# Kernel optimization log

Measured on AMD Instinct MI355X. Metric: run time of the kernel, lower is better.

## Reference

```python
import jax, jax.numpy as jnp
import numpy as np

B, C, H, W = 8, 512, 64, 64
CDIV = 8
CFG = C // CDIV  # f/g channels = 64


def setup_inputs() -> dict:
    key = jax.random.key(0)
    ks = jax.random.split(key, 8)
    x = jax.random.normal(ks[0], (B, C, H, W), dtype=jnp.float32)
    # 1x1 conv weights (spectral-norm omitted: weights used as-given), orthogonal-ish small init
    Wf = jax.random.normal(ks[1], (CFG, C), dtype=jnp.float32) * 0.02
    bf = jnp.zeros((CFG,), dtype=jnp.float32)
    Wg = jax.random.normal(ks[2], (CFG, C), dtype=jnp.float32) * 0.02
    bg = jnp.zeros((CFG,), dtype=jnp.float32)
    Wh = jax.random.normal(ks[3], (C, C), dtype=jnp.float32) * 0.02
    bh = jnp.zeros((C,), dtype=jnp.float32)
    # module inits gamma=0 (identity output); use 0.5 so the attention path is exercised
    gamma = jnp.float32(0.5)
    return {"x": x, "Wf": Wf, "bf": bf, "Wg": Wg, "bg": bg, "Wh": Wh, "bh": bh, "gamma": gamma}


def reference(x, Wf, bf, Wg, bg, Wh, bh, gamma):
    Bb, Cc, Hh, Ww = x.shape
    N = Hh * Ww
    xf = x.reshape(Bb, Cc, N)  # [B, C, N]
    # 1x1 convs == per-pixel linear maps
    f = jnp.einsum('oc,bcn->bon', Wf, xf) + bf[:, None]  # [B, CFG, N]
    g = jnp.einsum('oc,bcn->bon', Wg, xf) + bg[:, None]  # [B, CFG, N]
    h = jnp.einsum('oc,bcn->bon', Wh, xf) + bh[:, None]  # [B, C, N]
    # attention scores over spatial tokens: queries g, keys f -> [B, N, N]
    s = jnp.einsum('bci,bcj->bij', g, f)
    beta = jax.nn.softmax(s, axis=-1)
    o = jnp.einsum('bij,bcj->bci', beta, h).reshape(Bb, Cc, Hh, Ww)
    return gamma * o + x
```

## Files before the change

kernel.cpp:

```cpp
#include <hip/hip_runtime.h>
#include <hip/hip_bf16.h>

typedef __bf16 bf16;
typedef __attribute__((ext_vector_type(2))) __bf16 bf16x2;
typedef __attribute__((ext_vector_type(4))) __bf16 bf16x4;
typedef __attribute__((ext_vector_type(8))) __bf16 bf16x8;
typedef __attribute__((ext_vector_type(4))) float f32x4;
typedef long long i64;
typedef unsigned char u8;

#define MFMA16x16x32 __builtin_amdgcn_mfma_f32_16x16x32_bf16
#define MFMA_FP8 __builtin_amdgcn_mfma_f32_16x16x32_fp8_fp8

#define NB 8
#define NC 512
#define NN 4096
#define CFG 64

#define XP 520
#define TP 74

#define EXP_OFF 4.5f

__global__ __launch_bounds__(256) void k_wprep(
    const float* __restrict__ Wf, const float* __restrict__ bfv,
    const float* __restrict__ Wg, const float* __restrict__ bgv,
    const float* __restrict__ Wh,
    bf16* __restrict__ Wfg, bf16* __restrict__ Whb, float* __restrict__ bfg)
{
    int idx = blockIdx.x * 256 + threadIdx.x;
    if (idx < 32768)       Wfg[idx] = (bf16)Wf[idx];
    else if (idx < 65536)  Wfg[idx] = (bf16)Wg[idx - 32768];
    if (idx < 262144)      Whb[idx] = (bf16)Wh[idx];
    if (idx < 64)          bfg[idx] = bfv[idx];
    else if (idx < 128)    bfg[idx] = bgv[idx - 64];
}

__global__ __launch_bounds__(512) void k_fused(
    const float* __restrict__ x, const bf16* __restrict__ Wfg,
    const float* __restrict__ bfg, const bf16* __restrict__ Whb,
    const float* __restrict__ bh,
    bf16* __restrict__ fF, bf16* __restrict__ gF, u8* __restrict__ hT)
{
    __shared__ bf16 X[64 * XP];
    __shared__ bf16 tile[64 * TP];

    int b = blockIdx.x, n0 = blockIdx.y * 64;
    int t = threadIdx.x;

    for (int cc = 0; cc < 8; cc++) {
        int cl = t >> 3, seg = (t & 7) * 8;
        const float* src = x + ((size_t)(b * NC + cc * 64 + cl)) * NN + n0 + seg;
        float4 v0 = ((const float4*)src)[0];
        float4 v1 = ((const float4*)src)[1];
        bf16* tr = &tile[cl * TP + seg];
        *(bf16x2*)(tr + 0) = bf16x2{(bf16)v0.x, (bf16)v0.y};
        *(bf16x2*)(tr + 2) = bf16x2{(bf16)v0.z, (bf16)v0.w};
        *(bf16x2*)(tr + 4) = bf16x2{(bf16)v1.x, (bf16)v1.y};
        *(bf16x2*)(tr + 6) = bf16x2{(bf16)v1.z, (bf16)v1.w};
        __syncthreads();
        int nl = t >> 3, cs = (t & 7) * 8;
        bf16 buf[8];
#pragma unroll
        for (int u = 0; u < 8; u++) buf[u] = tile[(cs + u) * TP + nl];
        *(bf16x8*)&X[nl * XP + cc * 64 + cs] = *(bf16x8*)buf;
        __syncthreads();
    }

    int w = t >> 6, l = t & 63;
    int lr = l & 15, lq = l >> 4;

    {
        const bf16* Ab = Whb + (size_t)(w * 64) * NC;
        f32x4 acc[4][4] = {};
        for (int k0 = 0; k0 < NC; k0 += 32) {
            bf16x8 a[4], bb[4];
#pragma unroll
            for (int fi = 0; fi < 4; fi++)
                a[fi] = *(const bf16x8*)(Ab + (size_t)(fi*16 + lr) * NC + k0 + lq*8);
#pragma unroll
            for (int fj = 0; fj < 4; fj++)
                bb[fj] = *(const bf16x8*)&X[(fj*16 + lr) * XP + k0 + lq*8];
#pragma unroll
            for (int fi = 0; fi < 4; fi++)
#pragma unroll
                for (int fj = 0; fj < 4; fj++)
                    acc[fi][fj] = MFMA16x16x32(a[fi], bb[fj], acc[fi][fj], 0, 0, 0);
        }
#pragma unroll
        for (int fi = 0; fi < 4; fi++)
#pragma unroll
            for (int fj = 0; fj < 4; fj++)
#pragma unroll
                for (int tt = 0; tt < 4; tt++) {
                    int c = w*64 + fi*16 + lq*4 + tt;
                    int j = n0 + fj*16 + lr;
                    float v = acc[fi][fj][tt] + bh[c];
                    int jt = j >> 6, ks = (j >> 5) & 1, lqd = (j >> 3) & 3, e = j & 7;
                    int ct = c >> 4, crd = c & 15;
                    size_t off = ((((size_t)(b*64 + jt)*32 + ct)*2 + ks)*64 + (lqd*16 + crd))*8 + e;
                    int pk = __builtin_amdgcn_cvt_pk_fp8_f32(v, v, 0, false);
                    hT[off] = (u8)pk;
                }
    }

    {
        const bf16* Bb = Wfg + (size_t)(w * 16) * NC;
        f32x4 acc2[4] = {};
        for (int k0 = 0; k0 < NC; k0 += 32) {
            bf16x8 a[4], bo;
#pragma unroll
            for (int fi = 0; fi < 4; fi++)
                a[fi] = *(const bf16x8*)&X[(fi*16 + lr) * XP + k0 + lq*8];
            bo = *(const bf16x8*)(Bb + (size_t)lr * NC + k0 + lq*8);
#pragma unroll
            for (int fi = 0; fi < 4; fi++)
                acc2[fi] = MFMA16x16x32(a[fi], bo, acc2[fi], 0, 0, 0);
        }
#pragma unroll
        for (int fi = 0; fi < 4; fi++)
#pragma unroll
            for (int tt = 0; tt < 4; tt++) {
                int n = n0 + fi*16 + lq*4 + tt;
                int o = w*16 + lr;
                float v = acc2[fi][tt] + bfg[o];
                int c = o & 63;
                bf16* dst = (o < 64) ? fF : gF;
                int jt16 = n >> 4, nr = n & 15;
                int ks = c >> 5, lqd = (c >> 3) & 3, e = c & 7;
                size_t off = (((size_t)(b*256 + jt16)*2 + ks)*64 + (lqd*16 + nr))*8 + e;
                dst[off] = (bf16)v;
            }
    }
}

__global__ __launch_bounds__(1024, 4) void k_attn(
    const bf16* __restrict__ fF, const bf16* __restrict__ gF,
    const u8* __restrict__ hT, const float* __restrict__ x,
    const float* __restrict__ gammap, float* __restrict__ out)
{
    __shared__ alignas(16) u8 Pl[2][2][8192];
    __shared__ alignas(16) bf16 fS[2][8192];
    __shared__ float lpart[8][2][16];
    __shared__ alignas(16) float linv[128];

    int b  = blockIdx.x;
    int i0 = blockIdx.y * 128;
    int t = threadIdx.x;
    int w = t >> 6, l = t & 63;
    int lr = l & 15, lq = l >> 4;

    float gamma = *gammap;
    int fi_s = w >> 1;
    int ks_s = w & 1;

    u8* Pf = &Pl[0][0][0];
    int wrA = ((fi_s*2 + ks_s)*64 + (lq >> 1)*16 + lr)*8 + (lq & 1)*4;

    const bf16* gbase = gF + ((size_t)(b*256 + (i0 >> 4) + fi_s)*2)*512 + (size_t)l*8;
    bf16x8 bg0 = *(const bf16x8*)(gbase);
    bf16x8 bg1 = *(const bf16x8*)(gbase + 512);

    const bf16* fb0 = fF + (size_t)b*256*2*512;
    const u8* hb0 = hT + (size_t)b*2097152 + (size_t)(w*4)*512 + (size_t)l*8;

    f32x4 oacc[8][2] = {};
    float lsum = 0.f;

#define F_LOAD(q, reg)  { (reg) = *(const bf16x8*)(fb0 + (size_t)(q)*8192 + t*8); }
#define F_WRITE(q, reg) { *(bf16x8*)&fS[(q) & 1][t*8] = (reg); }

#define S_STEP(jn, fbuf, pbuf, slot)                                           \
    {                                                                          \
        const bf16* fb = &fS[fbuf][((jn) & 1)*4096 + ks_s*2048] + l*8;         \
        bf16x8 af00 = *(const bf16x8*)(fb);                                    \
        bf16x8 af01 = *(const bf16x8*)(fb + 512);                              \
        bf16x8 af10 = *(const bf16x8*)(fb + 1024);                             \
        bf16x8 af11 = *(const bf16x8*)(fb + 1536);                             \
        f32x4 s0 = {}, s1 = {};                                                \
        s0 = MFMA16x16x32(af00, bg0, s0, 0, 0, 0);                             \
        s0 = MFMA16x16x32(af01, bg1, s0, 0, 0, 0);                             \
        s1 = MFMA16x16x32(af10, bg0, s1, 0, 0, 0);                             \
        s1 = MFMA16x16x32(af11, bg1, s1, 0, 0, 0);                             \
        float e00 = __expf(s0[0] - EXP_OFF), e01 = __expf(s0[1] - EXP_OFF);    \
        float e02 = __expf(s0[2] - EXP_OFF), e03 = __expf(s0[3] - EXP_OFF);    \
        float e10 = __expf(s1[0] - EXP_OFF), e11 = __expf(s1[1] - EXP_OFF);    \
        float e12 = __expf(s1[2] - EXP_OFF), e13 = __expf(s1[3] - EXP_OFF);    \
        lsum += (e00 + e01 + e02 + e03) + (e10 + e11 + e12 + e13);             \
        int pk0 = __builtin_amdgcn_cvt_pk_fp8_f32(e00, e01, 0, false);         \
        pk0     = __builtin_amdgcn_cvt_pk_fp8_f32(e02, e03, pk0, true);        \
        int pk1 = __builtin_amdgcn_cvt_pk_fp8_f32(e10, e11, 0, false);         \
        pk1     = __builtin_amdgcn_cvt_pk_fp8_f32(e12, e13, pk1, true);        \
        *(int*)(Pf + ((pbuf)*2 + (slot))*8192 + wrA)       = pk0;              \
        *(int*)(Pf + ((pbuf)*2 + (slot))*8192 + wrA + 256) = pk1;              \
    }

#define PV_STEP(jt, pbuf, slot)                                                \
    {                                                                          \
        const u8* hb = hb0 + (size_t)(jt) * 32768;                             \
        i64 ah00 = *(const i64*)(hb);                                          \
        i64 ah01 = *(const i64*)(hb + 512);                                    \
        i64 ah10 = *(const i64*)(hb + 1024);                                   \
        i64 ah11 = *(const i64*)(hb + 1536);                                   \
        const u8* Pr = Pf + ((pbuf)*2 + (slot))*8192 + l*8;                    \
        __builtin_amdgcn_s_setprio(1);                                         \
        _Pragma("unroll")                                                      \
        for (int fi = 0; fi < 8; fi++) {                                       \
            i64 ap0 = *(const i64*)(Pr + (fi*2 + 0)*512);                      \
            i64 ap1 = *(const i64*)(Pr + (fi*2 + 1)*512);                      \
            oacc[fi][0] = MFMA_FP8(ap0, ah00, oacc[fi][0], 0, 0, 0);           \
            oacc[fi][0] = MFMA_FP8(ap1, ah01, oacc[fi][0], 0, 0, 0);           \
            oacc[fi][1] = MFMA_FP8(ap0, ah10, oacc[fi][1], 0, 0, 0);           \
            oacc[fi][1] = MFMA_FP8(ap1, ah11, oacc[fi][1], 0, 0, 0);           \
        }                                                                      \
        __builtin_amdgcn_s_setprio(0);                                         \
    }

    {
        bf16x8 fr;
        F_LOAD(0, fr)
        F_WRITE(0, fr)
        __syncthreads();
        F_LOAD(1, fr)
        S_STEP(0, 0, 0, 0)
        S_STEP(1, 0, 0, 1)
        F_WRITE(1, fr)
        __syncthreads();
    }

    for (int p = 0; p < 30; p++) {
        int cur = p & 1, nxt = cur ^ 1;

        bf16x8 fr;
        F_LOAD(p + 2, fr)

        PV_STEP(2*p,     cur, 0)
        PV_STEP(2*p + 1, cur, 1)

        S_STEP(2*p + 2, nxt, nxt, 0)
        S_STEP(2*p + 3, nxt, nxt, 1)

        F_WRITE(p + 2, fr)

        __syncthreads();
    }

    PV_STEP(60, 0, 0)
    PV_STEP(61, 0, 1)
    S_STEP(62, 1, 1, 0)
    S_STEP(63, 1, 1, 1)
    __syncthreads();
    PV_STEP(62, 1, 0)
    PV_STEP(63, 1, 1)

#undef S_STEP
#undef PV_STEP
#undef F_LOAD
#undef F_WRITE

    lsum += __shfl_xor(lsum, 16, 64);
    lsum += __shfl_xor(lsum, 32, 64);
    if (lq == 0) lpart[fi_s][ks_s][lr] = lsum;
    __syncthreads();
    if (t < 128) {
        linv[t] = 1.0f / (lpart[t >> 4][0][t & 15] + lpart[t >> 4][1][t & 15]);
    }
    __syncthreads();

    int cw = w * 32;
    const float* xb = x + (size_t)b * NC * NN;
    float* ob = out + (size_t)b * NC * NN;
#pragma unroll
    for (int fi = 0; fi < 8; fi++) {
        f32x4 li = *(const f32x4*)&linv[fi*16 + lq*4];
#pragma unroll
        for (int fc = 0; fc < 2; fc++) {
            int c = cw + fc*16 + lr;
            size_t base = (size_t)c * NN + i0 + fi*16 + lq*4;
            float4 xv = *(const float4*)(xb + base);
            float4 ov;
            ov.x = gamma * oacc[fi][fc][0] * li[0] + xv.x;
            ov.y = gamma * oacc[fi][fc][1] * li[1] + xv.y;
            ov.z = gamma * oacc[fi][fc][2] * li[2] + xv.z;
            ov.w = gamma * oacc[fi][fc][3] * li[3] + xv.w;
            *(float4*)(ob + base) = ov;
        }
    }
}

extern "C" void kernel_launch(void* const* d_in, const int* in_sizes, int n_in,
                              void* d_out, int out_size, void* d_ws, size_t ws_size,
                              hipStream_t stream)
{
    const float* x     = (const float*)d_in[0];
    const float* Wf    = (const float*)d_in[1];
    const float* bf_   = (const float*)d_in[2];
    const float* Wg    = (const float*)d_in[3];
    const float* bg_   = (const float*)d_in[4];
    const float* Wh    = (const float*)d_in[5];
    const float* bh_   = (const float*)d_in[6];
    const float* gamma = (const float*)d_in[7];
    float* out = (float*)d_out;

    char* ws = (char*)d_ws;
    u8*    hT  = (u8*)(ws + 33554432);
    bf16*  fF  = (bf16*)(ws + 67108864);
    bf16*  gF  = (bf16*)(ws + 71303168);
    bf16*  Wfg = (bf16*)(ws + 75497472);
    bf16*  Whb = (bf16*)(ws + 75628544);
    float* bfg = (float*)(ws + 76152832);

    k_wprep<<<dim3(1024), dim3(256), 0, stream>>>(Wf, bf_, Wg, bg_, Wh, Wfg, Whb, bfg);
    k_fused<<<dim3(8, 64), dim3(512), 0, stream>>>(x, Wfg, bfg, Whb, bh_, fF, gF, hT);
    k_attn<<<dim3(8, 32), dim3(1024), 0, stream>>>(fF, gF, hT, x, gamma, out);
}
```

Before: 188.4 us.

## Switch PV product to scaled 16x16x128 FP8 MFMA with wider K tiles

Replaces the 16x16x32 FP8 MFMAs in the P·V stage with the gfx950 scaled MFMA 16x16x128 f8f6f4 instruction, using unit scales. The hT layout written by the fused projection kernel and the P tile layout in LDS are reorganised so each lane feeds 32 contiguous bytes per operand, and one PV step now covers 128 keys. The aim is to cut MFMA issue count and the number of load instructions per key block. In exchange, register pressure rises from the wider operands, and the loads use a different access pattern that could change LDS bank conflicts.

```diff
diff --git a/kernel.cpp b/kernel.cpp
--- a/kernel.cpp
+++ b/kernel.cpp
@@ -6,11 +6,12 @@
 typedef __attribute__((ext_vector_type(4))) __bf16 bf16x4;
 typedef __attribute__((ext_vector_type(8))) __bf16 bf16x8;
 typedef __attribute__((ext_vector_type(4))) float f32x4;
-typedef long long i64;
+typedef __attribute__((ext_vector_type(8))) int i32x8;
 typedef unsigned char u8;
 
 #define MFMA16x16x32 __builtin_amdgcn_mfma_f32_16x16x32_bf16
-#define MFMA_FP8 __builtin_amdgcn_mfma_f32_16x16x32_fp8_fp8
+#define MFMA_MX(a, b, c, sa, sb) \
+    __builtin_amdgcn_mfma_scale_f32_16x16x128_f8f6f4((a), (b), (c), 0, 0, 0, (sa), 0, (sb))
 
 #define NB 8
 #define NC 512
@@ -21,6 +22,7 @@
 #define TP 74
 
 #define EXP_OFF 4.5f
+#define SCALE_ONE 0x7F7F7F7F
 
 __global__ __launch_bounds__(256) void k_wprep(
     const float* __restrict__ Wf, const float* __restrict__ bfv,
@@ -96,9 +98,10 @@
                     int c = w*64 + fi*16 + lq*4 + tt;
                     int j = n0 + fj*16 + lr;
                     float v = acc[fi][fj][tt] + bh[c];
-                    int jt = j >> 6, ks = (j >> 5) & 1, lqd = (j >> 3) & 3, e = j & 7;
-                    int ct = c >> 4, crd = c & 15;
-                    size_t off = ((((size_t)(b*64 + jt)*32 + ct)*2 + ks)*64 + (lqd*16 + crd))*8 + e;
+                    size_t tile128 = (size_t)(b*32 + (j >> 7));
+                    size_t ctile   = (size_t)(c >> 4);
+                    size_t lane    = (size_t)(((j >> 5) & 3)*16 + (c & 15));
+                    size_t off     = ((tile128*32 + ctile)*64 + lane)*32 + (size_t)(j & 31);
                     int pk = __builtin_amdgcn_cvt_pk_fp8_f32(v, v, 0, false);
                     hT[off] = (u8)pk;
                 }
@@ -139,7 +142,7 @@
     const u8* __restrict__ hT, const float* __restrict__ x,
     const float* __restrict__ gammap, float* __restrict__ out)
 {
-    __shared__ alignas(16) u8 Pl[2][2][8192];
+    __shared__ alignas(16) u8 Pl[2][16384];
     __shared__ alignas(16) bf16 fS[2][8192];
     __shared__ float lpart[8][2][16];
     __shared__ alignas(16) float linv[128];
@@ -153,16 +156,16 @@
     float gamma = *gammap;
     int fi_s = w >> 1;
     int ks_s = w & 1;
-
-    u8* Pf = &Pl[0][0][0];
-    int wrA = ((fi_s*2 + ks_s)*64 + (lq >> 1)*16 + lr)*8 + (lq & 1)*4;
+    const int sone = SCALE_ONE;
+
+    u8* Pf = &Pl[0][0];
 
     const bf16* gbase = gF + ((size_t)(b*256 + (i0 >> 4) + fi_s)*2)*512 + (size_t)l*8;
     bf16x8 bg0 = *(const bf16x8*)(gbase);
     bf16x8 bg1 = *(const bf16x8*)(gbase + 512);
 
     const bf16* fb0 = fF + (size_t)b*256*2*512;
-    const u8* hb0 = hT + (size_t)b*2097152 + (size_t)(w*4)*512 + (size_t)l*8;
+    const u8* hb0 = hT + (size_t)b*2097152 + (size_t)(w*2)*2048 + (size_t)l*32;
 
     f32x4 oacc[8][2] = {};
     float lsum = 0.f;
@@ -170,7 +173,7 @@
 #define F_LOAD(q, reg)  { (reg) = *(const bf16x8*)(fb0 + (size_t)(q)*8192 + t*8); }
 #define F_WRITE(q, reg) { *(bf16x8*)&fS[(q) & 1][t*8] = (reg); }
 
-#define S_STEP(jn, fbuf, pbuf, slot)                                           \
+#define S_STEP(jn, fbuf, pbuf)                                                 \
     {                                                                          \
         const bf16* fb = &fS[fbuf][((jn) & 1)*4096 + ks_s*2048] + l*8;         \
         bf16x8 af00 = *(const bf16x8*)(fb);                                    \
@@ -191,27 +194,24 @@
         pk0     = __builtin_amdgcn_cvt_pk_fp8_f32(e02, e03, pk0, true);        \
         int pk1 = __builtin_amdgcn_cvt_pk_fp8_f32(e10, e11, 0, false);         \
         pk1     = __builtin_amdgcn_cvt_pk_fp8_f32(e12, e13, pk1, true);        \
-        *(int*)(Pf + ((pbuf)*2 + (slot))*8192 + wrA)       = pk0;              \
-        *(int*)(Pf + ((pbuf)*2 + (slot))*8192 + wrA + 256) = pk1;              \
-    }
-
-#define PV_STEP(jt, pbuf, slot)                                                \
+        u8* pw = Pf + (pbuf)*16384 + fi_s*2048                                 \
+                 + ((((jn) & 1)*2 + ks_s)*16 + lr)*32 + lq*4;                  \
+        *(int*)(pw)      = pk0;                                                \
+        *(int*)(pw + 16) = pk1;                                                \
+    }
+
+#define PV_STEP(ph, pbuf)                                                      \
     {                                                                          \
-        const u8* hb = hb0 + (size_t)(jt) * 32768;                             \
-        i64 ah00 = *(const i64*)(hb);                                          \
-        i64 ah01 = *(const i64*)(hb + 512);                                    \
-        i64 ah10 = *(const i64*)(hb + 1024);                                   \
-        i64 ah11 = *(const i64*)(hb + 1536);                                   \
-        const u8* Pr = Pf + ((pbuf)*2 + (slot))*8192 + l*8;                    \
+        const u8* hb = hb0 + (size_t)(ph)*65536;                               \
+        i32x8 ah0 = *(const i32x8*)(hb);                                       \
+        i32x8 ah1 = *(const i32x8*)(hb + 2048);                                \
+        const u8* Pr = Pf + (pbuf)*16384 + l*32;                               \
         __builtin_amdgcn_s_setprio(1);                                         \
         _Pragma("unroll")                                                      \
         for (int fi = 0; fi < 8; fi++) {                                       \
-            i64 ap0 = *(const i64*)(Pr + (fi*2 + 0)*512);                      \
-            i64 ap1 = *(const i64*)(Pr + (fi*2 + 1)*512);                      \
-            oacc[fi][0] = MFMA_FP8(ap0, ah00, oacc[fi][0], 0, 0, 0);           \
-            oacc[fi][0] = MFMA_FP8(ap1, ah01, oacc[fi][0], 0, 0, 0);           \
-            oacc[fi][1] = MFMA_FP8(ap0, ah10, oacc[fi][1], 0, 0, 0);           \
-            oacc[fi][1] = MFMA_FP8(ap1, ah11, oacc[fi][1], 0, 0, 0);           \
+            i32x8 ap = *(const i32x8*)(Pr + fi*2048);                          \
+            oacc[fi][0] = MFMA_MX(ap, ah0, oacc[fi][0], sone, sone);           \
+            oacc[fi][1] = MFMA_MX(ap, ah1, oacc[fi][1], sone, sone);           \
         }                                                                      \
         __builtin_amdgcn_s_setprio(0);                                         \
     }
@@ -222,8 +222,8 @@
         F_WRITE(0, fr)
         __syncthreads();
         F_LOAD(1, fr)
-        S_STEP(0, 0, 0, 0)
-        S_STEP(1, 0, 0, 1)
+        S_STEP(0, 0, 0)
+        S_STEP(1, 0, 0)
         F_WRITE(1, fr)
         __syncthreads();
     }
@@ -234,24 +234,21 @@
         bf16x8 fr;
         F_LOAD(p + 2, fr)
 
-        PV_STEP(2*p,     cur, 0)
-        PV_STEP(2*p + 1, cur, 1)
-
-        S_STEP(2*p + 2, nxt, nxt, 0)
-        S_STEP(2*p + 3, nxt, nxt, 1)
+        PV_STEP(p, cur)
+
+        S_STEP(2*p + 2, nxt, nxt)
+        S_STEP(2*p + 3, nxt, nxt)
 
         F_WRITE(p + 2, fr)
 
         __syncthreads();
     }
 
-    PV_STEP(60, 0, 0)
-    PV_STEP(61, 0, 1)
-    S_STEP(62, 1, 1, 0)
-    S_STEP(63, 1, 1, 1)
+    PV_STEP(30, 0)
+    S_STEP(62, 1, 1)
+    S_STEP(63, 1, 1)
     __syncthreads();
-    PV_STEP(62, 1, 0)
-    PV_STEP(63, 1, 1)
+    PV_STEP(31, 1)
 
 #undef S_STEP
 #undef PV_STEP
```

After: 174.8 us. 7.2% less time.
